# Kernel optimization log

Hardware: AMD Instinct MI355X
Metric: run time of the kernel (lower is better)

## Reference

```python
import jax, jax.numpy as jnp
import numpy as np

DIM = 1024
HEADS = 16
NUM_EXPERTS = 8
TOP_K = 2
INNER = 4 * DIM
EPS = 1e-5
NEG = -1e9


def setup_inputs() -> dict:
    key = jax.random.key(0)
    ks = jax.random.split(key, 12)
    s = 0.02
    return {
        "x": jax.random.normal(ks[0], (4, 1024, DIM), dtype=jnp.float32),
        "qkv_w": jax.random.normal(ks[1], (DIM, 3 * DIM), dtype=jnp.float32) * s,
        "out_w": jax.random.normal(ks[2], (DIM, DIM), dtype=jnp.float32) * s,
        "out_b": jnp.zeros((DIM,), dtype=jnp.float32),
        "thresh": jnp.float32(-2.0),
        "ln1_g": jnp.ones((DIM,), dtype=jnp.float32),
        "ln1_b": jnp.zeros((DIM,), dtype=jnp.float32),
        "ln2_g": jnp.ones((DIM,), dtype=jnp.float32),
        "ln2_b": jnp.zeros((DIM,), dtype=jnp.float32),
        "gate_w": jax.random.normal(ks[3], (DIM, NUM_EXPERTS), dtype=jnp.float32) * s,
        "w1": jax.random.normal(ks[4], (NUM_EXPERTS, DIM, INNER), dtype=jnp.float32) * s,
        "b1": jnp.zeros((NUM_EXPERTS, INNER), dtype=jnp.float32),
        "w2": jax.random.normal(ks[5], (NUM_EXPERTS, INNER, DIM), dtype=jnp.float32) * s,
        "b2": jnp.zeros((NUM_EXPERTS, DIM), dtype=jnp.float32),
    }


def _layernorm(x, g, b):
    mu = jnp.mean(x, axis=-1, keepdims=True)
    var = jnp.mean(jnp.square(x - mu), axis=-1, keepdims=True)
    return (x - mu) * jax.lax.rsqrt(var + EPS) * g + b


def reference(x, qkv_w, out_w, out_b, thresh, ln1_g, ln1_b, ln2_g, ln2_b,
              gate_w, w1, b1, w2, b2):
    B, N, D = x.shape
    H = HEADS
    Dh = D // H
    scale = Dh ** -0.5

    # --- Sparse attention (pre-norm, eval mode: dropout off) ---
    h = _layernorm(x, ln1_g, ln1_b)
    qkv = h @ qkv_w                                   # [B,N,3D]
    q, k, v = jnp.split(qkv, 3, axis=-1)
    def heads(t):
        return t.reshape(B, N, H, Dh).transpose(0, 2, 1, 3)  # [B,H,N,Dh]
    q, k, v = heads(q), heads(k), heads(v)
    dots = jnp.einsum("bhid,bhjd->bhij", q, k) * scale
    dots = jnp.where(dots < thresh, jnp.float32(NEG), dots)  # learnable sparsity
    attn = jax.nn.softmax(dots, axis=-1)
    o = jnp.einsum("bhij,bhjd->bhid", attn, v)
    o = o.transpose(0, 2, 1, 3).reshape(B, N, D)
    x = x + o @ out_w + out_b

    # --- MoE FFN (pre-norm) ---
    h2 = _layernorm(x, ln2_g, ln2_b).reshape(-1, D)   # [T,D]
    T = h2.shape[0]
    logits = h2 @ gate_w                              # [T,E]
    probs = jax.nn.softmax(logits, axis=-1)
    aux_loss = NUM_EXPERTS * jnp.sum(probs.mean(0) * probs.sum(0))

    top_w, top_i = jax.lax.top_k(logits, TOP_K)       # [T,k]
    top_w = jax.nn.softmax(top_w, axis=-1)
    # dense combine weights: [T,E], zero for unselected experts
    combine = jnp.zeros((T, NUM_EXPERTS), dtype=h2.dtype)
    combine = combine.at[jnp.arange(T)[:, None], top_i].set(top_w)

    out = jnp.zeros_like(h2)
    for e in range(NUM_EXPERTS):
        y = jax.nn.gelu(h2 @ w1[e] + b1[e], approximate=False) @ w2[e] + b2[e]
        out = out + combine[:, e:e + 1] * y

    x = x + out.reshape(B, N, D)
    return x, aux_loss
```

## Files before the change

kernel.cpp:

```cpp
#include <hip/hip_runtime.h>
#include <math.h>

#define DIM 1024
#define THREE_DIM 3072
#define INNER 4096
#define NTOK 4096
#define NPAIR 8192
#define NEXP 8
#define MAXMB 72
#define PARTROWS (MAXMB*128)

typedef __attribute__((ext_vector_type(8))) short bf16x8;
typedef __attribute__((ext_vector_type(4))) float f32x4;

__device__ __forceinline__ unsigned short f2bf(float f){
    unsigned int x = __float_as_uint(f);
    unsigned int r = x + 0x7fffu + ((x >> 16) & 1u);
    return (unsigned short)(r >> 16);
}

__device__ __forceinline__ float bf2f(unsigned short u){
    return __uint_as_float(((unsigned int)u) << 16);
}

__device__ __forceinline__ unsigned short us4c(ushort4 v, int i){
    return i == 0 ? v.x : (i == 1 ? v.y : (i == 2 ? v.z : v.w));
}

__device__ __forceinline__ void glds16(const void* g, void* l){
    __builtin_amdgcn_global_load_lds(
        (const __attribute__((address_space(1))) void*)g,
        (__attribute__((address_space(3))) void*)l, 16, 0, 0);
}

__device__ __forceinline__ int xcd_swz(){
    int cpx = gridDim.x >> 3;
    return (blockIdx.x & 7) * cpx + (blockIdx.x >> 3);
}

template<int WRITE_BF>
__global__ __launch_bounds__(256)
void ln_kernel(const float* __restrict__ X, const float* __restrict__ g,
               const float* __restrict__ b, float* __restrict__ outF,
               unsigned short* __restrict__ outB)
{
    int row = blockIdx.x;
    int t = threadIdx.x;
    const float4 v = *((const float4*)(X + (size_t)row*DIM) + t);
    float s = v.x + v.y + v.z + v.w;
    #pragma unroll
    for (int m = 1; m < 64; m <<= 1) s += __shfl_xor(s, m, 64);
    __shared__ float red[8];
    int wid = t >> 6, lane = t & 63;
    if (lane == 0) red[wid] = s;
    __syncthreads();
    float mu = (red[0]+red[1]+red[2]+red[3]) * (1.0f/DIM);
    float dx = v.x-mu, dy = v.y-mu, dz = v.z-mu, dw = v.w-mu;
    float s2 = dx*dx + dy*dy + dz*dz + dw*dw;
    #pragma unroll
    for (int m = 1; m < 64; m <<= 1) s2 += __shfl_xor(s2, m, 64);
    if (lane == 0) red[4+wid] = s2;
    __syncthreads();
    float var = (red[4]+red[5]+red[6]+red[7]) * (1.0f/DIM);
    float inv = rsqrtf(var + 1e-5f);
    const float4 gg = *((const float4*)g + t);
    const float4 bb = *((const float4*)b + t);
    float y0 = dx*inv*gg.x + bb.x;
    float y1 = dy*inv*gg.y + bb.y;
    float y2 = dz*inv*gg.z + bb.z;
    float y3 = dw*inv*gg.w + bb.w;
    if (outF){
        float4 o; o.x=y0; o.y=y1; o.z=y2; o.w=y3;
        *((float4*)(outF + (size_t)row*DIM) + t) = o;
    }
    if (WRITE_BF){
        ushort4 u; u.x=f2bf(y0); u.y=f2bf(y1); u.z=f2bf(y2); u.w=f2bf(y3);
        *((ushort4*)(outB + (size_t)row*DIM) + t) = u;
    }
}

template<int MODE>
__global__ __launch_bounds__(256)
void gemm_bf(const unsigned short* __restrict__ A,
             const unsigned short* __restrict__ BT,
             int K, int N, int gnx,
             const float* __restrict__ bias, const float* __restrict__ resid,
             unsigned short* __restrict__ outB, float* __restrict__ outF)
{
    __shared__ __align__(16) unsigned short As[128*64];
    __shared__ __align__(16) unsigned short Bs[128*64];
    int fid = xcd_swz();
    int nx = fid % gnx, my = fid / gnx;
    int m0 = my * 128, n0 = nx * 128;
    int t = threadIdx.x, lane = t & 63, wid = t >> 6;
    size_t aoff[4], boff[4];
    #pragma unroll
    for (int it = 0; it < 4; ++it){
        int chunk = it*256 + wid*64 + lane;
        int r = chunk >> 3, c16 = chunk & 7;
        int c16s = c16 ^ (r & 7);
        aoff[it] = (size_t)(m0 + r)*K + (size_t)(c16s*8);
        boff[it] = (size_t)(n0 + r)*K + (size_t)(c16s*8);
    }
    int wm = wid >> 1, wn = wid & 1;
    f32x4 acc[4][4];
    #pragma unroll
    for (int mi = 0; mi < 4; ++mi)
        #pragma unroll
        for (int ni = 0; ni < 4; ++ni)
            #pragma unroll
            for (int q = 0; q < 4; ++q) acc[mi][ni][q] = 0.f;

    for (int k0 = 0; k0 < K; k0 += 64){
        __syncthreads();
        #pragma unroll
        for (int it = 0; it < 4; ++it){
            glds16(A  + aoff[it] + k0, As + (size_t)(it*256 + wid*64)*8);
            glds16(BT + boff[it] + k0, Bs + (size_t)(it*256 + wid*64)*8);
        }
        __syncthreads();
        bf16x8 af[4][2], bg[4][2];
        #pragma unroll
        for (int mi = 0; mi < 4; ++mi){
            int row = wm*64 + mi*16 + (lane & 15);
            #pragma unroll
            for (int ks = 0; ks < 2; ++ks){
                int cg = (ks*4 + (lane >> 4)) ^ (row & 7);
                af[mi][ks] = *(const bf16x8*)&As[row*64 + cg*8];
            }
        }
        #pragma unroll
        for (int ni = 0; ni < 4; ++ni){
            int row = wn*64 + ni*16 + (lane & 15);
            #pragma unroll
            for (int ks = 0; ks < 2; ++ks){
                int cg = (ks*4 + (lane >> 4)) ^ (row & 7);
                bg[ni][ks] = *(const bf16x8*)&Bs[row*64 + cg*8];
            }
        }
        #pragma unroll
        for (int ks = 0; ks < 2; ++ks)
            #pragma unroll
            for (int mi = 0; mi < 4; ++mi)
                #pragma unroll
                for (int ni = 0; ni < 4; ++ni)
                    acc[mi][ni] = __builtin_amdgcn_mfma_f32_16x16x32_bf16(
                                      af[mi][ks], bg[ni][ks], acc[mi][ni], 0, 0, 0);
    }
    #pragma unroll
    for (int mi = 0; mi < 4; ++mi){
        #pragma unroll
        for (int ni = 0; ni < 4; ++ni){
            int ccol = n0 + wn*64 + ni*16 + (lane & 15);
            #pragma unroll
            for (int j = 0; j < 4; ++j){
                int row = m0 + wm*64 + mi*16 + (lane >> 4)*4 + j;
                float v = acc[mi][ni][j];
                if (MODE == 0){
                    outB[(size_t)row*N + ccol] = f2bf(v);
                } else {
                    outF[(size_t)row*N + ccol] =
                        v + bias[ccol] + resid[(size_t)row*N + ccol];
                }
            }
        }
    }
}

__global__ __launch_bounds__(256)
void attn4_kernel(const unsigned short* __restrict__ qkv,
                  unsigned short* __restrict__ O,
                  const float* __restrict__ threshp)
{
    __shared__ __align__(16) unsigned short Qs[64*64];
    __shared__ __align__(16) unsigned short Ks[64*64];
    __shared__ __align__(16) unsigned short Vp[8*520];
    __shared__ __align__(16) unsigned short Ps[4*1024];

    int fid = xcd_swz();
    int qt = fid & 15, hh = (fid >> 4) & 15, bb = fid >> 8;
    int t = threadIdx.x, lane = t & 63, w = t >> 6;
    int arow = lane & 15, agrp = lane >> 4;
    int qrow0 = bb*1024 + qt*64;
    float thresh = threshp[0];

    #pragma unroll
    for (int it = 0; it < 2; ++it){
        int chunk = it*256 + w*64 + lane;
        int r = chunk >> 3, c16 = chunk & 7;
        glds16(qkv + (size_t)(qrow0+r)*3072 + hh*64 + ((c16 ^ (r & 7))*8),
               Qs + (size_t)(it*256 + w*64)*8);
    }
    __syncthreads();
    bf16x8 qf[2];
    {
        int row = w*16 + arow;
        #pragma unroll
        for (int s = 0; s < 2; ++s){
            int c = (s*4 + agrp) ^ (row & 7);
            qf[s] = *(const bf16x8*)&Qs[row*64 + c*8];
        }
    }

    float m_[4], l_[4];
    f32x4 acc[4];
    #pragma unroll
    for (int j = 0; j < 4; ++j){ m_[j] = -INFINITY; l_[j] = 0.f; }
    #pragma unroll
    for (int d4 = 0; d4 < 4; ++d4)
        #pragma unroll
        for (int j = 0; j < 4; ++j) acc[d4][j] = 0.f;

    for (int kt = 0; kt < 16; ++kt){
        __syncthreads();
        int krow0 = bb*1024 + kt*64;
        #pragma unroll
        for (int it = 0; it < 2; ++it){
            int chunk = it*256 + w*64 + lane;
            int r = chunk >> 3, c16 = chunk & 7;
            glds16(qkv + (size_t)(krow0+r)*3072 + 1024 + hh*64 + ((c16 ^ (r & 7))*8),
                   Ks + (size_t)(it*256 + w*64)*8);
        }
        if (t < 128){
            int jc = t & 7, d0 = (t >> 3) * 4;
            ushort4 u[8];
            #pragma unroll
            for (int jj = 0; jj < 8; ++jj)
                u[jj] = *(const ushort4*)(qkv + (size_t)(krow0 + jc*8 + jj)*3072
                                          + 2048 + hh*64 + d0);
            #pragma unroll
            for (int i = 0; i < 4; ++i){
                ushort4 a, b;
                a.x = us4c(u[0], i); a.y = us4c(u[1], i);
                a.z = us4c(u[2], i); a.w = us4c(u[3], i);
                b.x = us4c(u[4], i); b.y = us4c(u[5], i);
                b.z = us4c(u[6], i); b.w = us4c(u[7], i);
                *(ushort4*)&Vp[jc*520 + (d0+i)*8]     = a;
                *(ushort4*)&Vp[jc*520 + (d0+i)*8 + 4] = b;
            }
        }
        __syncthreads();

        f32x4 sv[4];
        #pragma unroll
        for (int n = 0; n < 4; ++n)
            #pragma unroll
            for (int j = 0; j < 4; ++j) sv[n][j] = 0.f;
        #pragma unroll
        for (int n = 0; n < 4; ++n){
            int krow = n*16 + arow;
            #pragma unroll
            for (int s = 0; s < 2; ++s){
                int c = (s*4 + agrp) ^ (krow & 7);
                bf16x8 kf = *(const bf16x8*)&Ks[krow*64 + c*8];
                sv[n] = __builtin_amdgcn_mfma_f32_16x16x32_bf16(qf[s], kf, sv[n], 0, 0, 0);
            }
        }
        #pragma unroll
        for (int n = 0; n < 4; ++n)
            #pragma unroll
            for (int j = 0; j < 4; ++j){
                float s = sv[n][j] * 0.125f;
                sv[n][j] = (s < thresh) ? -1e9f : s;
            }
        float tmax[4], fac[4], rsum[4];
        #pragma unroll
        for (int j = 0; j < 4; ++j)
            tmax[j] = fmaxf(fmaxf(sv[0][j], sv[1][j]), fmaxf(sv[2][j], sv[3][j]));
        #pragma unroll
        for (int msk = 1; msk < 16; msk <<= 1)
            #pragma unroll
            for (int j = 0; j < 4; ++j)
                tmax[j] = fmaxf(tmax[j], __shfl_xor(tmax[j], msk, 64));
        #pragma unroll
        for (int j = 0; j < 4; ++j){
            float mn = fmaxf(m_[j], tmax[j]);
            fac[j] = __expf(m_[j] - mn);
            m_[j] = mn;
        }
        #pragma unroll
        for (int n = 0; n < 4; ++n)
            #pragma unroll
            for (int j = 0; j < 4; ++j)
                sv[n][j] = __expf(sv[n][j] - m_[j]);
        #pragma unroll
        for (int j = 0; j < 4; ++j)
            rsum[j] = sv[0][j] + sv[1][j] + sv[2][j] + sv[3][j];
        #pragma unroll
        for (int msk = 1; msk < 16; msk <<= 1)
            #pragma unroll
            for (int j = 0; j < 4; ++j)
                rsum[j] += __shfl_xor(rsum[j], msk, 64);
        #pragma unroll
        for (int j = 0; j < 4; ++j)
            l_[j] = l_[j]*fac[j] + rsum[j];
        #pragma unroll
        for (int n = 0; n < 4; ++n){
            int col = n*16 + arow;
            #pragma unroll
            for (int j = 0; j < 4; ++j){
                int r = agrp*4 + j;
                int idx = r*64 + (((col>>3) ^ (r&7)) << 3) + (col & 7);
                Ps[w*1024 + idx] = f2bf(sv[n][j]);
            }
        }
        #pragma unroll
        for (int d4 = 0; d4 < 4; ++d4)
            #pragma unroll
            for (int j = 0; j < 4; ++j) acc[d4][j] *= fac[j];
        #pragma unroll
        for (int s = 0; s < 2; ++s){
            int c = (s*4 + agrp) ^ (arow & 7);
            bf16x8 pa = *(const bf16x8*)&Ps[w*1024 + arow*64 + c*8];
            int jc = s*4 + agrp;
            #pragma unroll
            for (int d4 = 0; d4 < 4; ++d4){
                int dcol = d4*16 + arow;
                bf16x8 vb = *(const bf16x8*)&Vp[jc*520 + dcol*8];
                acc[d4] = __builtin_amdgcn_mfma_f32_16x16x32_bf16(pa, vb, acc[d4], 0, 0, 0);
            }
        }
    }
    #pragma unroll
    for (int j = 0; j < 4; ++j){
        float inv = 1.0f / l_[j];
        int row = qrow0 + w*16 + agrp*4 + j;
        #pragma unroll
        for (int d4 = 0; d4 < 4; ++d4)
            O[(size_t)row*1024 + hh*64 + d4*16 + arow] = f2bf(acc[d4][j] * inv);
    }
}

__global__ __launch_bounds__(64)
void gate_kernel(const float* __restrict__ h2, const float* __restrict__ gw,
                 float* __restrict__ probs, int* __restrict__ top_i,
                 float* __restrict__ top_w)
{
    int tk = blockIdx.x;
    int lane = threadIdx.x;
    const float* hr = h2 + (size_t)tk*DIM;
    float acc[8];
    #pragma unroll
    for (int e = 0; e < 8; ++e) acc[e] = 0.f;
    for (int d = lane; d < DIM; d += 64){
        float hv = hr[d];
        const float* grow = gw + d*8;
        #pragma unroll
        for (int e = 0; e < 8; ++e) acc[e] = fmaf(hv, grow[e], acc[e]);
    }
    #pragma unroll
    for (int m = 1; m < 64; m <<= 1)
        #pragma unroll
        for (int e = 0; e < 8; ++e) acc[e] += __shfl_xor(acc[e], m, 64);
    if (lane == 0){
        float mx = acc[0];
        #pragma unroll
        for (int e = 1; e < 8; ++e) mx = fmaxf(mx, acc[e]);
        float p[8], s = 0.f;
        #pragma unroll
        for (int e = 0; e < 8; ++e){ p[e] = __expf(acc[e]-mx); s += p[e]; }
        float invs = 1.f/s;
        #pragma unroll
        for (int e = 0; e < 8; ++e) probs[(size_t)tk*8+e] = p[e]*invs;
        int i0 = 0; float v0 = acc[0];
        #pragma unroll
        for (int e = 1; e < 8; ++e) if (acc[e] > v0){ v0 = acc[e]; i0 = e; }
        int i1 = -1; float v1 = -INFINITY;
        #pragma unroll
        for (int e = 0; e < 8; ++e) if (e != i0 && acc[e] > v1){ v1 = acc[e]; i1 = e; }
        float w0 = 1.f/(1.f + __expf(v1 - v0));
        top_i[tk*2]   = i0; top_i[tk*2+1] = i1;
        top_w[tk*2]   = w0; top_w[tk*2+1] = 1.f - w0;
    }
}

__global__ __launch_bounds__(256)
void aux_kernel(const float* __restrict__ probs, float* __restrict__ dout)
{
    int t = threadIdx.x;
    float acc[8];
    #pragma unroll
    for (int e = 0; e < 8; ++e) acc[e] = 0.f;
    for (int r = t; r < NTOK; r += 256){
        const float* pr = probs + (size_t)r*8;
        #pragma unroll
        for (int e = 0; e < 8; ++e) acc[e] += pr[e];
    }
    #pragma unroll
    for (int m = 1; m < 64; m <<= 1)
        #pragma unroll
        for (int e = 0; e < 8; ++e) acc[e] += __shfl_xor(acc[e], m, 64);
    __shared__ float red[4][8];
    int wid = t >> 6, lane = t & 63;
    if (lane == 0)
        for (int e = 0; e < 8; ++e) red[wid][e] = acc[e];
    __syncthreads();
    if (t == 0){
        float aux = 0.f;
        for (int e = 0; e < 8; ++e){
            float S = red[0][e]+red[1][e]+red[2][e]+red[3][e];
            aux += S*S;
        }
        dout[(size_t)NTOK*DIM] = aux * (8.0f/NTOK);
    }
}

__global__ __launch_bounds__(512)
void routing_kernel(const int* __restrict__ topi, int* __restrict__ perm,
                    int* __restrict__ mblk_e, int* __restrict__ tokslot)
{
    __shared__ int cnt[8];
    __shared__ int obase[8];
    int t = threadIdx.x, w = t >> 6, lane = t & 63;
    int c = 0;
    for (int i0 = 0; i0 < NPAIR; i0 += 64){
        int e = topi[i0 + lane];
        c += (e == w) ? 1 : 0;
    }
    #pragma unroll
    for (int m = 1; m < 64; m <<= 1) c += __shfl_xor(c, m, 64);
    if (lane == 0) cnt[w] = c;
    __syncthreads();
    if (t == 0){
        int mb = 0;
        for (int e = 0; e < 8; ++e){
            obase[e] = mb*128;
            int nb = (cnt[e] + 127) >> 7;
            for (int k = 0; k < nb; ++k) mblk_e[mb++] = e;
        }
        for (; mb < MAXMB; ++mb) mblk_e[mb] = -1;
    }
    __syncthreads();
    for (int i = t; i < MAXMB*128; i += 512) perm[i] = -1;
    __syncthreads();
    int base = obase[w];
    for (int i0 = 0; i0 < NPAIR; i0 += 64){
        int p = i0 + lane;
        int e = topi[p];
        bool mt = (e == w);
        unsigned long long mk = __ballot(mt);
        int rank = __popcll(mk & ((1ull << lane) - 1ull));
        if (mt){
            perm[base + rank] = p;
            tokslot[p] = base + rank;
        }
        base += __popcll(mk);
    }
}

template<int MODE>
__global__ __launch_bounds__(512, 4)
void gemm_moe3(const unsigned short* __restrict__ Abase,
               const unsigned short* __restrict__ BTbase,
               int K, int N, int lda,
               const int* __restrict__ perm, const int* __restrict__ mblk_e,
               const float* __restrict__ bias,
               unsigned short* __restrict__ actout,
               unsigned short* __restrict__ partout)
{
    const int GNX = (MODE == 2) ? (INNER/256) : (DIM/256);
    int fid = xcd_swz();
    int nx = fid % GNX;
    int rest = fid / GNX;
    int mb = rest % MAXMB;
    int kk = rest / MAXMB;
    int e = mblk_e[mb];
    if (e < 0) return;
    int kspan = (MODE == 2) ? K : (K >> 1);
    int kbeg = kk * kspan, kend = kbeg + kspan;

    __shared__ __align__(16) unsigned short As[128*64];
    __shared__ __align__(16) unsigned short Bs[256*64];
    __shared__ int permL[128];
    int t = threadIdx.x;
    if (MODE == 2 && t < 128) permL[t] = perm[mb*128 + t];
    __syncthreads();
    int lane = t & 63, wid = t >> 6;
    int wm = wid >> 2, wn = wid & 3;
    int n0 = nx * 256;
    const unsigned short* BT = BTbase + (size_t)e * (size_t)N * (size_t)K;
    size_t aoff[2], boff[4];
    #pragma unroll
    for (int it = 0; it < 2; ++it){
        int chunk = it*512 + t;
        int r = chunk >> 3, c16 = chunk & 7;
        int c16s = c16 ^ (r & 7);
        size_t ar;
        if (MODE == 2){ int p = permL[r]; ar = (p >= 0) ? (size_t)(p >> 1) : 0; }
        else          { ar = (size_t)(mb*128 + r); }
        aoff[it] = ar*(size_t)lda + (size_t)(c16s*8);
    }
    #pragma unroll
    for (int it = 0; it < 4; ++it){
        int chunk = it*512 + t;
        int r = chunk >> 3, c16 = chunk & 7;
        int c16s = c16 ^ (r & 7);
        boff[it] = (size_t)(n0 + r)*(size_t)K + (size_t)(c16s*8);
    }
    f32x4 acc[4][4];
    #pragma unroll
    for (int mi = 0; mi < 4; ++mi)
        #pragma unroll
        for (int ni = 0; ni < 4; ++ni)
            #pragma unroll
            for (int q = 0; q < 4; ++q) acc[mi][ni][q] = 0.f;

    for (int k0 = kbeg; k0 < kend; k0 += 64){
        __syncthreads();
        #pragma unroll
        for (int it = 0; it < 2; ++it)
            glds16(Abase + aoff[it] + k0, As + (size_t)(it*512 + wid*64)*8);
        #pragma unroll
        for (int it = 0; it < 4; ++it)
            glds16(BT    + boff[it] + k0, Bs + (size_t)(it*512 + wid*64)*8);
        __syncthreads();
        #pragma unroll
        for (int ks = 0; ks < 2; ++ks){
            bf16x8 af[4], bg[4];
            #pragma unroll
            for (int mi = 0; mi < 4; ++mi){
                int row = wm*64 + mi*16 + (lane & 15);
                int cg = (ks*4 + (lane >> 4)) ^ (row & 7);
                af[mi] = *(const bf16x8*)&As[row*64 + cg*8];
            }
            #pragma unroll
            for (int ni = 0; ni < 4; ++ni){
                int row = wn*64 + ni*16 + (lane & 15);
                int cg = (ks*4 + (lane >> 4)) ^ (row & 7);
                bg[ni] = *(const bf16x8*)&Bs[row*64 + cg*8];
            }
            #pragma unroll
            for (int mi = 0; mi < 4; ++mi)
                #pragma unroll
                for (int ni = 0; ni < 4; ++ni)
                    acc[mi][ni] = __builtin_amdgcn_mfma_f32_16x16x32_bf16(
                                      af[mi], bg[ni], acc[mi][ni], 0, 0, 0);
        }
    }
    #pragma unroll
    for (int mi = 0; mi < 4; ++mi){
        #pragma unroll
        for (int ni = 0; ni < 4; ++ni){
            int ccol = n0 + wn*64 + ni*16 + (lane & 15);
            float bv = (kk == 0) ? bias[(size_t)e*N + ccol] : 0.f;
            #pragma unroll
            for (int j = 0; j < 4; ++j){
                int rloc = wm*64 + mi*16 + (lane >> 4)*4 + j;
                float v = acc[mi][ni][j];
                if (MODE == 2){
                    float gx = v + bv;
                    float z2 = gx * fmaf(gx*gx, 0.07135481283f, 1.595769122f);
                    float ex = __expf(-z2);
                    float gl = gx * __builtin_amdgcn_rcpf(1.0f + ex);
                    actout[(size_t)(mb*128 + rloc)*N + ccol] = f2bf(gl);
                } else {
                    partout[((size_t)kk*PARTROWS + mb*128 + rloc)*N + ccol] = f2bf(v + bv);
                }
            }
        }
    }
}

__global__ __launch_bounds__(256)
void combine_kernel(const unsigned short* __restrict__ part,
                    const int* __restrict__ tokslot,
                    const float* __restrict__ topw,
                    float* __restrict__ out)
{
    int tk = blockIdx.x, t = threadIdx.x;
    int s0 = tokslot[tk*2], s1 = tokslot[tk*2+1];
    float w0 = topw[tk*2], w1 = topw[tk*2+1];
    ushort4 a0 = *((const ushort4*)(part + (size_t)s0*DIM) + t);
    ushort4 a1 = *((const ushort4*)(part + ((size_t)PARTROWS + s0)*DIM) + t);
    ushort4 b0 = *((const ushort4*)(part + (size_t)s1*DIM) + t);
    ushort4 b1 = *((const ushort4*)(part + ((size_t)PARTROWS + s1)*DIM) + t);
    float4* o4 = (float4*)(out + (size_t)tk*DIM) + t;
    float4 o = *o4;
    o.x += w0*(bf2f(a0.x) + bf2f(a1.x)) + w1*(bf2f(b0.x) + bf2f(b1.x));
    o.y += w0*(bf2f(a0.y) + bf2f(a1.y)) + w1*(bf2f(b0.y) + bf2f(b1.y));
    o.z += w0*(bf2f(a0.z) + bf2f(a1.z)) + w1*(bf2f(b0.z) + bf2f(b1.z));
    o.w += w0*(bf2f(a0.w) + bf2f(a1.w)) + w1*(bf2f(b0.w) + bf2f(b1.w));
    *o4 = o;
}

__global__ __launch_bounds__(256)
void transp_cast(const float* __restrict__ W, unsigned short* __restrict__ WT,
                 int K, int N)
{
    __shared__ float tile[32][33];
    size_t base = (size_t)blockIdx.z * (size_t)K * (size_t)N;
    const float* Wp = W + base;
    unsigned short* Tp = WT + base;
    int t = threadIdx.x;
    int r = t >> 3, c4 = (t & 7) << 2;
    int n0 = blockIdx.x << 5, k0 = blockIdx.y << 5;
    float4 v = *(const float4*)(Wp + (size_t)(k0+r)*N + n0 + c4);
    tile[r][c4+0] = v.x; tile[r][c4+1] = v.y;
    tile[r][c4+2] = v.z; tile[r][c4+3] = v.w;
    __syncthreads();
    ushort4 u;
    u.x = f2bf(tile[c4+0][r]);
    u.y = f2bf(tile[c4+1][r]);
    u.z = f2bf(tile[c4+2][r]);
    u.w = f2bf(tile[c4+3][r]);
    *(ushort4*)(Tp + (size_t)(n0+r)*K + k0 + c4) = u;
}

extern "C" void kernel_launch(void* const* d_in, const int* in_sizes, int n_in,
                              void* d_out, int out_size, void* d_ws, size_t ws_size,
                              hipStream_t stream)
{
    const float* x      = (const float*)d_in[0];
    const float* qkv_w  = (const float*)d_in[1];
    const float* out_w  = (const float*)d_in[2];
    const float* out_b  = (const float*)d_in[3];
    const float* thresh = (const float*)d_in[4];
    const float* ln1_g  = (const float*)d_in[5];
    const float* ln1_b  = (const float*)d_in[6];
    const float* ln2_g  = (const float*)d_in[7];
    const float* ln2_b  = (const float*)d_in[8];
    const float* gate_w = (const float*)d_in[9];
    const float* w1     = (const float*)d_in[10];
    const float* b1     = (const float*)d_in[11];
    const float* w2     = (const float*)d_in[12];
    const float* b2     = (const float*)d_in[13];
    float* out = (float*)d_out;
    char* ws = (char*)d_ws;

    const size_t MB = (size_t)1 << 20;
    unsigned short* h1bf  = (unsigned short*)(ws);
    unsigned short* qkvbf = (unsigned short*)(ws + 8*MB);
    unsigned short* obf   = (unsigned short*)(ws + 32*MB);
    float*          h2    = (float*)(ws + 40*MB);
    unsigned short* h2bf  = (unsigned short*)(ws + 56*MB);
    unsigned short* qwT   = (unsigned short*)(ws + 64*MB);
    unsigned short* owT   = (unsigned short*)(ws + 70*MB);
    unsigned short* w1T   = (unsigned short*)(ws + 72*MB);
    unsigned short* w2T   = (unsigned short*)(ws + 136*MB);
    unsigned short* act   = (unsigned short*)(ws + 200*MB);
    float* probs          = (float*)(ws + 276*MB);
    int*   top_i          = (int*)(ws + 276*MB + 131072);
    float* top_w          = (float*)(ws + 276*MB + 163840);
    int*   perm           = (int*)(ws + 276*MB + 196608);
    int*   mblk           = (int*)(ws + 276*MB + 237568);
    int*   tokslot        = (int*)(ws + 276*MB + 241664);
    unsigned short* part  = (unsigned short*)(ws + 280*MB);

    transp_cast<<<dim3(THREE_DIM/32, DIM/32, 1), 256, 0, stream>>>(qkv_w, qwT, DIM, THREE_DIM);
    transp_cast<<<dim3(DIM/32, DIM/32, 1), 256, 0, stream>>>(out_w, owT, DIM, DIM);

    ln_kernel<1><<<NTOK, 256, 0, stream>>>(x, ln1_g, ln1_b, nullptr, h1bf);
    gemm_bf<0><<<(THREE_DIM/128)*(NTOK/128), 256, 0, stream>>>(
        h1bf, qwT, DIM, THREE_DIM, THREE_DIM/128, nullptr, nullptr, qkvbf, nullptr);
    attn4_kernel<<<16*16*4, 256, 0, stream>>>(qkvbf, obf, thresh);
    gemm_bf<1><<<(DIM/128)*(NTOK/128), 256, 0, stream>>>(
        obf, owT, DIM, DIM, DIM/128, out_b, x, nullptr, out);
    ln_kernel<1><<<NTOK, 256, 0, stream>>>(out, ln2_g, ln2_b, h2, h2bf);
    gate_kernel<<<NTOK, 64, 0, stream>>>(h2, gate_w, probs, top_i, top_w);
    aux_kernel<<<1, 256, 0, stream>>>(probs, out);
    routing_kernel<<<1, 512, 0, stream>>>(top_i, perm, mblk, tokslot);

    transp_cast<<<dim3(INNER/32, DIM/32, NEXP), 256, 0, stream>>>(w1, w1T, DIM, INNER);
    transp_cast<<<dim3(DIM/32, INNER/32, NEXP), 256, 0, stream>>>(w2, w2T, INNER, DIM);

    gemm_moe3<2><<<(INNER/256)*MAXMB, 512, 0, stream>>>(
        h2bf, w1T, DIM, INNER, DIM, perm, mblk, b1, act, nullptr);
    gemm_moe3<3><<<(DIM/256)*MAXMB*2, 512, 0, stream>>>(
        act, w2T, INNER, DIM, INNER, perm, mblk, b2, nullptr, part);
    combine_kernel<<<NTOK, 256, 0, stream>>>(part, tokslot, top_w, out);
}
```

Before: 510.1 us.

## Run MoE expert GEMMs in FP8 with FP8 weights and activations

Converts the expert weights, the post-LN2 activations and the intermediate GELU activations to FP8 (e4m3) instead of bf16. Both expert GEMMs now use the fp8 MFMA instruction, with a reworked LDS tile layout and swizzle for 1-byte elements, and the launch bounds are raised to allow more resident waves. The goal is to halve operand memory traffic and use the higher-throughput FP8 matrix path. The cost is a large loss of precision: small weights around 0.02 land near e4m3's subnormal range, so the output may drift from the reference.

```diff
diff --git a/kernel.cpp b/kernel.cpp
--- a/kernel.cpp
+++ b/kernel.cpp
@@ -12,6 +12,7 @@
 
 typedef __attribute__((ext_vector_type(8))) short bf16x8;
 typedef __attribute__((ext_vector_type(4))) float f32x4;
+typedef long fp8x8;
 
 __device__ __forceinline__ unsigned short f2bf(float f){
     unsigned int x = __float_as_uint(f);
@@ -27,6 +28,17 @@
     return i == 0 ? v.x : (i == 1 ? v.y : (i == 2 ? v.z : v.w));
 }
 
+__device__ __forceinline__ unsigned int f4fp8(float a, float b, float c, float d){
+    int p = __builtin_amdgcn_cvt_pk_fp8_f32(a, b, 0, false);
+    p = __builtin_amdgcn_cvt_pk_fp8_f32(c, d, p, true);
+    return (unsigned int)p;
+}
+
+__device__ __forceinline__ unsigned char f2fp8(float f){
+    int p = __builtin_amdgcn_cvt_pk_fp8_f32(f, f, 0, false);
+    return (unsigned char)(p & 0xff);
+}
+
 __device__ __forceinline__ void glds16(const void* g, void* l){
     __builtin_amdgcn_global_load_lds(
         (const __attribute__((address_space(1))) void*)g,
@@ -38,11 +50,11 @@
     return (blockIdx.x & 7) * cpx + (blockIdx.x >> 3);
 }
 
-template<int WRITE_BF>
 __global__ __launch_bounds__(256)
 void ln_kernel(const float* __restrict__ X, const float* __restrict__ g,
                const float* __restrict__ b, float* __restrict__ outF,
-               unsigned short* __restrict__ outB)
+               unsigned short* __restrict__ outB,
+               unsigned char* __restrict__ outF8)
 {
     int row = blockIdx.x;
     int t = threadIdx.x;
@@ -73,9 +85,12 @@
         float4 o; o.x=y0; o.y=y1; o.z=y2; o.w=y3;
         *((float4*)(outF + (size_t)row*DIM) + t) = o;
     }
-    if (WRITE_BF){
+    if (outB){
         ushort4 u; u.x=f2bf(y0); u.y=f2bf(y1); u.z=f2bf(y2); u.w=f2bf(y3);
         *((ushort4*)(outB + (size_t)row*DIM) + t) = u;
+    }
+    if (outF8){
+        *((unsigned int*)(outF8 + (size_t)row*DIM) + t) = f4fp8(y0, y1, y2, y3);
     }
 }
 
@@ -449,13 +464,13 @@
 }
 
 template<int MODE>
-__global__ __launch_bounds__(512, 4)
-void gemm_moe3(const unsigned short* __restrict__ Abase,
-               const unsigned short* __restrict__ BTbase,
+__global__ __launch_bounds__(512, 8)
+void gemm_moe8(const unsigned char* __restrict__ Abase,
+               const unsigned char* __restrict__ BTbase,
                int K, int N, int lda,
                const int* __restrict__ perm, const int* __restrict__ mblk_e,
                const float* __restrict__ bias,
-               unsigned short* __restrict__ actout,
+               unsigned char* __restrict__ actout,
                unsigned short* __restrict__ partout)
 {
     const int GNX = (MODE == 2) ? (INNER/256) : (DIM/256);
@@ -469,8 +484,8 @@
     int kspan = (MODE == 2) ? K : (K >> 1);
     int kbeg = kk * kspan, kend = kbeg + kspan;
 
-    __shared__ __align__(16) unsigned short As[128*64];
-    __shared__ __align__(16) unsigned short Bs[256*64];
+    __shared__ __align__(16) unsigned char As[128*64];
+    __shared__ __align__(16) unsigned char Bs[256*64];
     __shared__ int permL[128];
     int t = threadIdx.x;
     if (MODE == 2 && t < 128) permL[t] = perm[mb*128 + t];
@@ -478,24 +493,24 @@
     int lane = t & 63, wid = t >> 6;
     int wm = wid >> 2, wn = wid & 3;
     int n0 = nx * 256;
-    const unsigned short* BT = BTbase + (size_t)e * (size_t)N * (size_t)K;
-    size_t aoff[2], boff[4];
-    #pragma unroll
-    for (int it = 0; it < 2; ++it){
-        int chunk = it*512 + t;
-        int r = chunk >> 3, c16 = chunk & 7;
-        int c16s = c16 ^ (r & 7);
+    const unsigned char* BT = BTbase + (size_t)e * (size_t)N * (size_t)K;
+    size_t aoff;
+    {
+        int chunk = t;
+        int r = chunk >> 2, c16 = chunk & 3;
+        int c16s = c16 ^ (r & 3);
         size_t ar;
         if (MODE == 2){ int p = permL[r]; ar = (p >= 0) ? (size_t)(p >> 1) : 0; }
         else          { ar = (size_t)(mb*128 + r); }
-        aoff[it] = ar*(size_t)lda + (size_t)(c16s*8);
-    }
-    #pragma unroll
-    for (int it = 0; it < 4; ++it){
+        aoff = ar*(size_t)lda + (size_t)(c16s*16);
+    }
+    size_t boff[2];
+    #pragma unroll
+    for (int it = 0; it < 2; ++it){
         int chunk = it*512 + t;
-        int r = chunk >> 3, c16 = chunk & 7;
-        int c16s = c16 ^ (r & 7);
-        boff[it] = (size_t)(n0 + r)*(size_t)K + (size_t)(c16s*8);
+        int r = chunk >> 2, c16 = chunk & 3;
+        int c16s = c16 ^ (r & 3);
+        boff[it] = (size_t)(n0 + r)*(size_t)K + (size_t)(c16s*16);
     }
     f32x4 acc[4][4];
     #pragma unroll
@@ -507,33 +522,33 @@
 
     for (int k0 = kbeg; k0 < kend; k0 += 64){
         __syncthreads();
+        glds16(Abase + aoff + k0, As + (size_t)(wid*64 + lane)*16);
         #pragma unroll
         for (int it = 0; it < 2; ++it)
-            glds16(Abase + aoff[it] + k0, As + (size_t)(it*512 + wid*64)*8);
-        #pragma unroll
-        for (int it = 0; it < 4; ++it)
-            glds16(BT    + boff[it] + k0, Bs + (size_t)(it*512 + wid*64)*8);
+            glds16(BT + boff[it] + k0, Bs + (size_t)(it*512 + wid*64 + lane)*16);
         __syncthreads();
         #pragma unroll
         for (int ks = 0; ks < 2; ++ks){
-            bf16x8 af[4], bg[4];
+            fp8x8 af[4], bg[4];
             #pragma unroll
             for (int mi = 0; mi < 4; ++mi){
                 int row = wm*64 + mi*16 + (lane & 15);
-                int cg = (ks*4 + (lane >> 4)) ^ (row & 7);
-                af[mi] = *(const bf16x8*)&As[row*64 + cg*8];
+                int o = ks*4 + (lane >> 4);
+                int lc = (o >> 1) ^ (row & 3);
+                af[mi] = *(const fp8x8*)&As[row*64 + lc*16 + (o & 1)*8];
             }
             #pragma unroll
             for (int ni = 0; ni < 4; ++ni){
                 int row = wn*64 + ni*16 + (lane & 15);
-                int cg = (ks*4 + (lane >> 4)) ^ (row & 7);
-                bg[ni] = *(const bf16x8*)&Bs[row*64 + cg*8];
+                int o = ks*4 + (lane >> 4);
+                int lc = (o >> 1) ^ (row & 3);
+                bg[ni] = *(const fp8x8*)&Bs[row*64 + lc*16 + (o & 1)*8];
             }
             #pragma unroll
             for (int mi = 0; mi < 4; ++mi)
                 #pragma unroll
                 for (int ni = 0; ni < 4; ++ni)
-                    acc[mi][ni] = __builtin_amdgcn_mfma_f32_16x16x32_bf16(
+                    acc[mi][ni] = __builtin_amdgcn_mfma_f32_16x16x32_fp8_fp8(
                                       af[mi], bg[ni], acc[mi][ni], 0, 0, 0);
         }
     }
@@ -552,7 +567,7 @@
                     float z2 = gx * fmaf(gx*gx, 0.07135481283f, 1.595769122f);
                     float ex = __expf(-z2);
                     float gl = gx * __builtin_amdgcn_rcpf(1.0f + ex);
-                    actout[(size_t)(mb*128 + rloc)*N + ccol] = f2bf(gl);
+                    actout[(size_t)(mb*128 + rloc)*N + ccol] = f2fp8(gl);
                 } else {
                     partout[((size_t)kk*PARTROWS + mb*128 + rloc)*N + ccol] = f2bf(v + bv);
                 }
@@ -604,6 +619,25 @@
     u.z = f2bf(tile[c4+2][r]);
     u.w = f2bf(tile[c4+3][r]);
     *(ushort4*)(Tp + (size_t)(n0+r)*K + k0 + c4) = u;
+}
+
+__global__ __launch_bounds__(256)
+void transp_cast8(const float* __restrict__ W, unsigned char* __restrict__ WT,
+                  int K, int N)
+{
+    __shared__ float tile[32][33];
+    size_t base = (size_t)blockIdx.z * (size_t)K * (size_t)N;
+    const float* Wp = W + base;
+    unsigned char* Tp = WT + base;
+    int t = threadIdx.x;
+    int r = t >> 3, c4 = (t & 7) << 2;
+    int n0 = blockIdx.x << 5, k0 = blockIdx.y << 5;
+    float4 v = *(const float4*)(Wp + (size_t)(k0+r)*N + n0 + c4);
+    tile[r][c4+0] = v.x; tile[r][c4+1] = v.y;
+    tile[r][c4+2] = v.z; tile[r][c4+3] = v.w;
+    __syncthreads();
+    unsigned int u = f4fp8(tile[c4+0][r], tile[c4+1][r], tile[c4+2][r], tile[c4+3][r]);
+    *(unsigned int*)(Tp + (size_t)(n0+r)*K + k0 + c4) = u;
 }
 
 extern "C" void kernel_launch(void* const* d_in, const int* in_sizes, int n_in,
@@ -632,12 +666,12 @@
     unsigned short* qkvbf = (unsigned short*)(ws + 8*MB);
     unsigned short* obf   = (unsigned short*)(ws + 32*MB);
     float*          h2    = (float*)(ws + 40*MB);
-    unsigned short* h2bf  = (unsigned short*)(ws + 56*MB);
+    unsigned char*  h2f8  = (unsigned char*)(ws + 56*MB);
     unsigned short* qwT   = (unsigned short*)(ws + 64*MB);
     unsigned short* owT   = (unsigned short*)(ws + 70*MB);
-    unsigned short* w1T   = (unsigned short*)(ws + 72*MB);
-    unsigned short* w2T   = (unsigned short*)(ws + 136*MB);
-    unsigned short* act   = (unsigned short*)(ws + 200*MB);
+    unsigned char*  w1T8  = (unsigned char*)(ws + 72*MB);
+    unsigned char*  w2T8  = (unsigned char*)(ws + 104*MB);
+    unsigned char*  act8  = (unsigned char*)(ws + 136*MB);
     float* probs          = (float*)(ws + 276*MB);
     int*   top_i          = (int*)(ws + 276*MB + 131072);
     float* top_w          = (float*)(ws + 276*MB + 163840);
@@ -649,23 +683,23 @@
     transp_cast<<<dim3(THREE_DIM/32, DIM/32, 1), 256, 0, stream>>>(qkv_w, qwT, DIM, THREE_DIM);
     transp_cast<<<dim3(DIM/32, DIM/32, 1), 256, 0, stream>>>(out_w, owT, DIM, DIM);
 
-    ln_kernel<1><<<NTOK, 256, 0, stream>>>(x, ln1_g, ln1_b, nullptr, h1bf);
+    ln_kernel<<<NTOK, 256, 0, stream>>>(x, ln1_g, ln1_b, nullptr, h1bf, nullptr);
     gemm_bf<0><<<(THREE_DIM/128)*(NTOK/128), 256, 0, stream>>>(
         h1bf, qwT, DIM, THREE_DIM, THREE_DIM/128, nullptr, nullptr, qkvbf, nullptr);
     attn4_kernel<<<16*16*4, 256, 0, stream>>>(qkvbf, obf, thresh);
     gemm_bf<1><<<(DIM/128)*(NTOK/128), 256, 0, stream>>>(
         obf, owT, DIM, DIM, DIM/128, out_b, x, nullptr, out);
-    ln_kernel<1><<<NTOK, 256, 0, stream>>>(out, ln2_g, ln2_b, h2, h2bf);
+    ln_kernel<<<NTOK, 256, 0, stream>>>(out, ln2_g, ln2_b, h2, nullptr, h2f8);
     gate_kernel<<<NTOK, 64, 0, stream>>>(h2, gate_w, probs, top_i, top_w);
     aux_kernel<<<1, 256, 0, stream>>>(probs, out);
     routing_kernel<<<1, 512, 0, stream>>>(top_i, perm, mblk, tokslot);
 
-    transp_cast<<<dim3(INNER/32, DIM/32, NEXP), 256, 0, stream>>>(w1, w1T, DIM, INNER);
-    transp_cast<<<dim3(DIM/32, INNER/32, NEXP), 256, 0, stream>>>(w2, w2T, INNER, DIM);
-
-    gemm_moe3<2><<<(INNER/256)*MAXMB, 512, 0, stream>>>(
-        h2bf, w1T, DIM, INNER, DIM, perm, mblk, b1, act, nullptr);
-    gemm_moe3<3><<<(DIM/256)*MAXMB*2, 512, 0, stream>>>(
-        act, w2T, INNER, DIM, INNER, perm, mblk, b2, nullptr, part);
+    transp_cast8<<<dim3(INNER/32, DIM/32, NEXP), 256, 0, stream>>>(w1, w1T8, DIM, INNER);
+    transp_cast8<<<dim3(DIM/32, INNER/32, NEXP), 256, 0, stream>>>(w2, w2T8, INNER, DIM);
+
+    gemm_moe8<2><<<(INNER/256)*MAXMB, 512, 0, stream>>>(
+        h2f8, w1T8, DIM, INNER, DIM, perm, mblk, b1, act8, nullptr);
+    gemm_moe8<3><<<(DIM/256)*MAXMB*2, 512, 0, stream>>>(
+        act8, w2T8, INNER, DIM, INNER, perm, mblk, b2, nullptr, part);
     combine_kernel<<<NTOK, 256, 0, stream>>>(part, tokslot, top_w, out);
 }
```

New measurement: 1.546 ms. +203.1%, slower.
